# Kernel optimization log

Measured on AMD Instinct MI355X. Metric: run time of the kernel, lower is better.

Reference implementation:

```python
import jax, jax.numpy as jnp
import numpy as np

NUM_HEADS = 12
HEAD_CH = 64
WINDOW = 4


def _relative_to_absolute(x):
    # x: (B, H, L, 2L-1) -> (B, H, L, L) via skew trick
    B, H, L, _ = x.shape
    x = jnp.pad(x, ((0, 0), (0, 0), (0, 0), (0, 1)))        # (B,H,L,2L)
    x = x.reshape(B, H, L * 2 * L)
    x = jnp.pad(x, ((0, 0), (0, 0), (0, L - 1)))
    x = x.reshape(B, H, L + 1, 2 * L - 1)
    return x[:, :, :L, L - 1:]


def _get_relative_embeddings(emb, L):
    # emb: (H, 2W+1, D) -> (H, 2L-1, D)
    pad = max(0, L - WINDOW - 1)
    start = max(0, WINDOW - L + 1)
    e = jnp.pad(emb, ((0, 0), (pad, pad), (0, 0)))
    return e[:, start:start + 2 * L - 1, :]


def _forward(x, wq, bq, wk, bk, wv, bv, wo, bo, emb_rel_k, emb_rel_v):
    B, C, L = x.shape
    H, D = NUM_HEADS, HEAD_CH
    scale = 1.0 / np.sqrt(D).astype(np.float32)

    # 1x1 conv == channel matmul
    q = jnp.einsum('oc,bcl->bol', wq, x) + bq[None, :, None]
    k = jnp.einsum('oc,bcl->bol', wk, x) + bk[None, :, None]
    v = jnp.einsum('oc,bcl->bol', wv, x) + bv[None, :, None]

    # (B, C, L) -> (B, H, L, D)
    q = q.reshape(B, H, D, L).transpose(0, 1, 3, 2)
    k = k.reshape(B, H, D, L).transpose(0, 1, 3, 2)
    v = v.reshape(B, H, D, L).transpose(0, 1, 3, 2)

    score = jnp.einsum('bhld,bhmd->bhlm', q, k) * scale      # (B,H,L,L)

    rel_k = _get_relative_embeddings(emb_rel_k, L)           # (H, 2L-1, D)
    s_rel = jnp.einsum('bhld,hmd->bhlm', q, rel_k)           # (B,H,L,2L-1)
    score = score + _relative_to_absolute(s_rel) * scale

    attn = jax.nn.softmax(score, axis=-1)                    # dropout p=0 -> identity

    res = jnp.einsum('bhlm,bhmd->bhld', attn, v)             # (B,H,L,D)

    # absolute_to_relative skew
    a = jnp.pad(attn, ((0, 0), (0, 0), (0, 0), (0, L - 1)))
    a = a.reshape(B, H, L * (2 * L - 1))
    a = jnp.pad(a, ((0, 0), (0, 0), (L, 0)))
    rel_w = a.reshape(B, H, L, 2 * L)[:, :, :, 1:]           # (B,H,L,2L-1)

    rel_v = _get_relative_embeddings(emb_rel_v, L)           # (H, 2L-1, D)
    res = res + jnp.einsum('bhlm,hmd->bhld', rel_w, rel_v)

    res = res.transpose(0, 1, 3, 2).reshape(B, H * D, L)     # (B, C, L)
    out = jnp.einsum('oc,bcl->bol', wo, res) + bo[None, :, None]
    return out


def setup_inputs() -> dict:
    key = jax.random.key(0)
    ks = jax.random.split(key, 11)
    B, C, L = 4, 768, 1024
    rel_std = HEAD_CH ** (-0.5)
    xavier = np.sqrt(6.0 / (C + C)).astype(np.float32)
    return {
        'x': jax.random.normal(ks[0], (B, C, L), jnp.float32),
        'wq': jax.random.uniform(ks[1], (C, C), jnp.float32, -xavier, xavier),
        'bq': jnp.zeros((C,), jnp.float32),
        'wk': jax.random.uniform(ks[2], (C, C), jnp.float32, -xavier, xavier),
        'bk': jnp.zeros((C,), jnp.float32),
        'wv': jax.random.uniform(ks[3], (C, C), jnp.float32, -xavier, xavier),
        'bv': jnp.zeros((C,), jnp.float32),
        'wo': jax.random.normal(ks[4], (C, C), jnp.float32) * 0.02,
        'bo': jnp.zeros((C,), jnp.float32),
        'emb_rel_k': jax.random.normal(ks[5], (NUM_HEADS, 2 * WINDOW + 1, HEAD_CH), jnp.float32) * rel_std,
        'emb_rel_v': jax.random.normal(ks[6], (NUM_HEADS, 2 * WINDOW + 1, HEAD_CH), jnp.float32) * rel_std,
    }


def reference(x, wq, bq, wk, bk, wv, bv, wo, bo, emb_rel_k, emb_rel_v):
    return _forward(x, wq, bq, wk, bk, wv, bv, wo, bo, emb_rel_k, emb_rel_v)
```

## Files before the change

kernel.cpp:

```cpp
#include <hip/hip_runtime.h>

#define NB   4
#define NH   12
#define HD   64
#define CCH  768
#define LQ   1024
#define SCALE 0.125f
#define STAB  4.0f
#define WELE (CCH*CCH)

typedef unsigned short u16;
typedef __bf16 bf16x8 __attribute__((ext_vector_type(8)));
typedef unsigned short u16x8 __attribute__((ext_vector_type(8)));
typedef unsigned short u16x4 __attribute__((ext_vector_type(4)));
typedef float floatx4 __attribute__((ext_vector_type(4)));

__device__ __forceinline__ float bf2f(u16 u) {
    union { unsigned int i; float f; } x; x.i = ((unsigned int)u) << 16; return x.f;
}
__device__ __forceinline__ u16 f2bf_u(float f) {
    union { float f; unsigned int i; } x; x.f = f;
    unsigned int i = x.i;
    return (u16)((i + 0x7FFFu + ((i >> 16) & 1u)) >> 16);
}
__device__ __forceinline__ void glds16(const u16* g, u16* l) {
    __builtin_amdgcn_global_load_lds(
        (const __attribute__((address_space(1))) unsigned int*)g,
        (__attribute__((address_space(3))) unsigned int*)l, 16, 0, 0);
}

__global__ __launch_bounds__(256) void convert_w_kernel(
    const float* __restrict__ wq, const float* __restrict__ wk,
    const float* __restrict__ wv, const float* __restrict__ wo,
    u16* __restrict__ wb)
{
    const int p = blockIdx.y;
    const float* src = (p == 0) ? wq : (p == 1) ? wk : (p == 2) ? wv : wo;
    u16* dst = wb + (size_t)p * WELE;
    const int idx = (blockIdx.x * 256 + threadIdx.x) * 4;
    const float4 v = *reinterpret_cast<const float4*>(src + idx);
    u16x4 o;
    o[0] = f2bf_u(v.x); o[1] = f2bf_u(v.y); o[2] = f2bf_u(v.z); o[3] = f2bf_u(v.w);
    *reinterpret_cast<u16x4*>(dst + idx) = o;
}

__global__ __launch_bounds__(256) void transpose_x_kernel(
    const float* __restrict__ x, u16* __restrict__ xT)
{
    __shared__ u16 tile[64 * 68];
    const int l0 = blockIdx.x * 64, c0 = blockIdx.y * 64, b = blockIdx.z;
    const int t = threadIdx.x;
    const float* xb = x + (size_t)b * CCH * LQ;
    {
        const int l = t & 63, cg = t >> 6;
        for (int i = 0; i < 16; ++i) {
            const int c = cg * 16 + i;
            tile[c * 68 + l] = f2bf_u(xb[(size_t)(c0 + c) * LQ + l0 + l]);
        }
    }
    __syncthreads();
    {
        const int c = t & 63, lg = t >> 6;
        for (int i = 0; i < 16; ++i) {
            const int l = lg * 16 + i;
            xT[((size_t)b * LQ + l0 + l) * CCH + c0 + c] = tile[c * 68 + l];
        }
    }
}

#define GEMM_CORE(Ag, Bg)                                                     \
    __shared__ __align__(16) u16 a_tile[128 * 64];                            \
    __shared__ __align__(16) u16 b_tile[128 * 64];                            \
    const int t = threadIdx.x;                                                \
    const int wave = t >> 6, lane = t & 63;                                   \
    const int quad = lane >> 4, l16 = lane & 15;                              \
    const int wm = (wave >> 1) * 64, wn = (wave & 1) * 64;                    \
    floatx4 acc[4][4];                                                        \
    _Pragma("unroll") for (int mi = 0; mi < 4; ++mi)                          \
        _Pragma("unroll") for (int ni = 0; ni < 4; ++ni)                      \
            _Pragma("unroll") for (int r = 0; r < 4; ++r) acc[mi][ni][r] = 0.f;\
    for (int k0 = 0; k0 < CCH; k0 += 64) {                                    \
        __syncthreads();                                                      \
        _Pragma("unroll") for (int i = 0; i < 4; ++i) {                       \
            const int sbase = wave * 256 + i * 64;                            \
            const int s = sbase + lane;                                       \
            const int m = s >> 3, pos = s & 7;                                \
            const int gpos = pos ^ (m & 7);                                   \
            glds16(Ag + (size_t)(m0 + m) * CCH + k0 + gpos * 8,               \
                   &a_tile[sbase * 8]);                                       \
            glds16(Bg + (size_t)(n0 + m) * CCH + k0 + gpos * 8,               \
                   &b_tile[sbase * 8]);                                       \
        }                                                                     \
        __syncthreads();                                                      \
        bf16x8 af[2][4], bfr[2][4];                                           \
        _Pragma("unroll") for (int s = 0; s < 2; ++s)                         \
            _Pragma("unroll") for (int i = 0; i < 4; ++i) {                   \
                const int am = wm + i * 16 + l16;                             \
                const int bn = wn + i * 16 + l16;                             \
                const int c = s * 4 + quad;                                   \
                af[s][i]  = *reinterpret_cast<const bf16x8*>(                 \
                    &a_tile[(am * 8 + (c ^ (am & 7))) * 8]);                  \
                bfr[s][i] = *reinterpret_cast<const bf16x8*>(                 \
                    &b_tile[(bn * 8 + (c ^ (bn & 7))) * 8]);                  \
            }                                                                 \
        _Pragma("unroll") for (int s = 0; s < 2; ++s)                         \
            _Pragma("unroll") for (int mi = 0; mi < 4; ++mi)                  \
                _Pragma("unroll") for (int ni = 0; ni < 4; ++ni)              \
                    acc[mi][ni] = __builtin_amdgcn_mfma_f32_16x16x32_bf16(    \
                        af[s][mi], bfr[s][ni], acc[mi][ni], 0, 0, 0);         \
    }

__global__ __launch_bounds__(256) void proj_qkv_kernel(
    const u16* __restrict__ xT, const u16* __restrict__ wb,
    const float* __restrict__ bq, const float* __restrict__ bk,
    const float* __restrict__ bv,
    u16* __restrict__ Qw, u16* __restrict__ Kw, u16* __restrict__ Vw)
{
    const int z = blockIdx.z, b = z / 3, p = z % 3;
    const int n0 = blockIdx.x * 128, m0 = blockIdx.y * 128;
    const u16* Ag = wb + (size_t)p * WELE;
    const u16* Bg = xT + (size_t)b * LQ * CCH;
    const float* bias = (p == 0) ? bq : (p == 1) ? bk : bv;
    u16* Y = ((p == 0) ? Qw : (p == 1) ? Kw : Vw) + (size_t)b * CCH * LQ;

    GEMM_CORE(Ag, Bg)

#pragma unroll
    for (int mi = 0; mi < 4; ++mi) {
#pragma unroll
        for (int r = 0; r < 4; ++r) {
            const int o = m0 + wm + mi * 16 + quad * 4 + r;
            const float bb = bias[o];
#pragma unroll
            for (int ni = 0; ni < 4; ++ni) {
                const int l = n0 + wn + ni * 16 + l16;
                Y[(size_t)o * LQ + l] = f2bf_u(acc[mi][ni][r] + bb);
            }
        }
    }
}

__global__ __launch_bounds__(256) void proj_out_kernel(
    const u16* __restrict__ resb, const u16* __restrict__ wb,
    const float* __restrict__ bo, float* __restrict__ out)
{
    const int b = blockIdx.z;
    const int n0 = blockIdx.x * 128, m0 = blockIdx.y * 128;
    const u16* Ag = wb + (size_t)3 * WELE;
    const u16* Bg = resb + (size_t)b * LQ * CCH;
    float* Y = out + (size_t)b * CCH * LQ;

    GEMM_CORE(Ag, Bg)

#pragma unroll
    for (int mi = 0; mi < 4; ++mi) {
#pragma unroll
        for (int r = 0; r < 4; ++r) {
            const int o = m0 + wm + mi * 16 + quad * 4 + r;
            const float bb = bo[o];
#pragma unroll
            for (int ni = 0; ni < 4; ++ni) {
                const int l = n0 + wn + ni * 16 + l16;
                Y[(size_t)o * LQ + l] = acc[mi][ni][r] + bb;
            }
        }
    }
}

#define KSTRIDE 72

__global__ __launch_bounds__(256) void attn_kernel(
    const u16* __restrict__ Qw, const u16* __restrict__ Kw,
    const u16* __restrict__ Vw,
    const float* __restrict__ erk, const float* __restrict__ erv,
    u16* __restrict__ resb)
{
    __shared__ __align__(16) u16 kv_lds[2 * 64 * KSTRIDE];
    __shared__ __align__(16) u16 p_lds[4 * 16 * KSTRIDE];
    __shared__ float bias_lds[64 * 9];
    __shared__ float bandw_lds[64 * 9];
    __shared__ float erk_lds[9 * 64];
    __shared__ float erv_lds[9 * 64];

    u16* k16 = kv_lds;
    u16* v16 = kv_lds + 64 * KSTRIDE;
    u16* kdiag = kv_lds;

    const int t = threadIdx.x;
    const int wave = t >> 6, lane = t & 63;
    const int quad = lane >> 4, l16 = lane & 15;
    const int l0 = blockIdx.x * 64, h = blockIdx.y, b = blockIdx.z;
    const int rbase = wave * 16;
    const size_t base = ((size_t)b * CCH + (size_t)h * HD) * LQ;
    const u16* Qb = Qw + base;
    const u16* Kb = Kw + base;
    const u16* Vb = Vw + base;

    for (int i = t; i < 9 * 64; i += 256) {
        erk_lds[i] = erk[(size_t)h * 9 * 64 + i];
        erv_lds[i] = erv[(size_t)h * 9 * 64 + i];
    }

    bf16x8 qa0, qa1;
    {
        const int lg = l0 + rbase + l16;
        union { u16x8 u; bf16x8 v; } t0, t1;
#pragma unroll
        for (int jj = 0; jj < 8; ++jj) {
            t0.u[jj] = Qb[(size_t)(quad * 8 + jj) * LQ + lg];
            t1.u[jj] = Qb[(size_t)(32 + quad * 8 + jj) * LQ + lg];
        }
        qa0 = t0.v; qa1 = t1.v;
    }
    __syncthreads();

    {
        union { bf16x8 v; u16x8 u; } a0, a1; a0.v = qa0; a1.v = qa1;
        float qf[16];
#pragma unroll
        for (int jj = 0; jj < 8; ++jj) { qf[jj] = bf2f(a0.u[jj]); qf[8 + jj] = bf2f(a1.u[jj]); }
        for (int dl = 0; dl < 9; ++dl) {
            float s = 0.f;
#pragma unroll
            for (int jj = 0; jj < 8; ++jj) {
                s += qf[jj]     * erk_lds[dl * 64 + quad * 8 + jj];
                s += qf[8 + jj] * erk_lds[dl * 64 + 32 + quad * 8 + jj];
            }
            s += __shfl_xor(s, 16, 64);
            s += __shfl_xor(s, 32, 64);
            if (quad == 0) bias_lds[(rbase + l16) * 9 + dl] = s;
        }
    }

    floatx4 O[4];
    float l_acc = 0.f;
#pragma unroll
    for (int i = 0; i < 4; ++i)
#pragma unroll
        for (int r = 0; r < 4; ++r) O[i][r] = 0.f;

    u16* pw = p_lds + wave * 16 * KSTRIDE;
    const int qrow = rbase + l16;
    const int lgq = l0 + qrow;

    for (int kb = 0; kb < 16; ++kb) {
        const int j0 = kb * 64;
        __syncthreads();
        {
            u16 tmp[16];
#pragma unroll
            for (int dd = 0; dd < 16; ++dd)
                tmp[dd] = Kb[(size_t)(wave * 16 + dd) * LQ + j0 + lane];
            *reinterpret_cast<u16x8*>(&k16[lane * KSTRIDE + wave * 16])     = *reinterpret_cast<u16x8*>(tmp);
            *reinterpret_cast<u16x8*>(&k16[lane * KSTRIDE + wave * 16 + 8]) = *reinterpret_cast<u16x8*>(tmp + 8);
        }
        {
            const int d = t >> 2, seg = t & 3;
            const u16x8* src = reinterpret_cast<const u16x8*>(Vb + (size_t)d * LQ + j0 + seg * 16);
            *reinterpret_cast<u16x8*>(&v16[d * KSTRIDE + seg * 16])     = src[0];
            *reinterpret_cast<u16x8*>(&v16[d * KSTRIDE + seg * 16 + 8]) = src[1];
        }
        __syncthreads();

        floatx4 s4[4];
#pragma unroll
        for (int tt = 0; tt < 4; ++tt) {
            const bf16x8 ka0 = *reinterpret_cast<const bf16x8*>(&k16[(tt * 16 + l16) * KSTRIDE + quad * 8]);
            const bf16x8 ka1 = *reinterpret_cast<const bf16x8*>(&k16[(tt * 16 + l16) * KSTRIDE + 32 + quad * 8]);
            floatx4 c;
#pragma unroll
            for (int r = 0; r < 4; ++r) c[r] = 0.f;
            c = __builtin_amdgcn_mfma_f32_16x16x32_bf16(ka0, qa0, c, 0, 0, 0);
            c = __builtin_amdgcn_mfma_f32_16x16x32_bf16(ka1, qa1, c, 0, 0, 0);
            s4[tt] = c;
        }

        {
            const int lgmin = l0 + rbase, lgmax = lgmin + 15;
            if (j0 + 63 >= lgmin - 4 && j0 <= lgmax + 4) {
#pragma unroll
                for (int tt = 0; tt < 4; ++tt) {
#pragma unroll
                    for (int r = 0; r < 4; ++r) {
                        const int key = j0 + tt * 16 + quad * 4 + r;
                        const int delta = key - lgq + 4;
                        if (delta >= 0 && delta <= 8) s4[tt][r] += bias_lds[qrow * 9 + delta];
                    }
                }
            }
        }

#pragma unroll
        for (int tt = 0; tt < 4; ++tt) {
            u16x4 pk;
#pragma unroll
            for (int r = 0; r < 4; ++r) {
                const float p = __expf(fmaf(s4[tt][r], SCALE, -STAB));
                l_acc += p;
                pk[r] = f2bf_u(p);
            }
            *reinterpret_cast<u16x4*>(&pw[l16 * KSTRIDE + tt * 16 + quad * 4]) = pk;
        }

        const bf16x8 pa0 = *reinterpret_cast<const bf16x8*>(&pw[l16 * KSTRIDE + quad * 8]);
        const bf16x8 pa1 = *reinterpret_cast<const bf16x8*>(&pw[l16 * KSTRIDE + 32 + quad * 8]);
#pragma unroll
        for (int tt = 0; tt < 4; ++tt) {
            const bf16x8 vb0 = *reinterpret_cast<const bf16x8*>(&v16[(tt * 16 + l16) * KSTRIDE + quad * 8]);
            const bf16x8 vb1 = *reinterpret_cast<const bf16x8*>(&v16[(tt * 16 + l16) * KSTRIDE + 32 + quad * 8]);
            O[tt] = __builtin_amdgcn_mfma_f32_16x16x32_bf16(pa0, vb0, O[tt], 0, 0, 0);
            O[tt] = __builtin_amdgcn_mfma_f32_16x16x32_bf16(pa1, vb1, O[tt], 0, 0, 0);
        }
    }

    float l_tot = l_acc;
    l_tot += __shfl_xor(l_tot, 16, 64);
    l_tot += __shfl_xor(l_tot, 32, 64);

    __syncthreads();

    {
#pragma unroll
        for (int dd = 0; dd < 16; ++dd) {
            const int d = wave * 16 + dd;
            int j = l0 - 4 + lane;
            int jc = min(max(j, 0), LQ - 1);
            kdiag[lane * KSTRIDE + d] = Kb[(size_t)d * LQ + jc];
            if (lane < 8) {
                j = l0 + 60 + lane;
                jc = min(j, LQ - 1);
                kdiag[(64 + lane) * KSTRIDE + d] = Kb[(size_t)d * LQ + jc];
            }
        }
    }
    __syncthreads();

    {
        union { bf16x8 v; u16x8 u; } a0, a1; a0.v = qa0; a1.v = qa1;
        float qf[16];
#pragma unroll
        for (int jj = 0; jj < 8; ++jj) { qf[jj] = bf2f(a0.u[jj]); qf[8 + jj] = bf2f(a1.u[jj]); }
        for (int dl = 0; dl < 9; ++dl) {
            union { bf16x8 v; u16x8 u; } k0, k1;
            k0.v = *reinterpret_cast<const bf16x8*>(&kdiag[(qrow + dl) * KSTRIDE + quad * 8]);
            k1.v = *reinterpret_cast<const bf16x8*>(&kdiag[(qrow + dl) * KSTRIDE + 32 + quad * 8]);
            float s = 0.f;
#pragma unroll
            for (int jj = 0; jj < 8; ++jj) {
                s += qf[jj]     * bf2f(k0.u[jj]);
                s += qf[8 + jj] * bf2f(k1.u[jj]);
            }
            s += __shfl_xor(s, 16, 64);
            s += __shfl_xor(s, 32, 64);
            const int jgl = lgq + dl - 4;
            float pband = 0.f;
            if (jgl >= 0 && jgl < LQ)
                pband = __expf(fmaf(s + bias_lds[qrow * 9 + dl], SCALE, -STAB));
            if (quad == 0) bandw_lds[qrow * 9 + dl] = pband;
        }
    }

    float rinv[4];
#pragma unroll
    for (int r = 0; r < 4; ++r) {
        const int src = (lane & 48) | (quad * 4 + r);
        rinv[r] = 1.0f / __shfl(l_tot, src, 64);
    }

#pragma unroll
    for (int tt = 0; tt < 4; ++tt) {
#pragma unroll
        for (int r = 0; r < 4; ++r) {
            const int row = rbase + quad * 4 + r;
            const int d = tt * 16 + l16;
            float val = O[tt][r];
#pragma unroll
            for (int dl = 0; dl < 9; ++dl)
                val += bandw_lds[row * 9 + dl] * erv_lds[dl * 64 + d];
            val *= rinv[r];
            resb[((size_t)b * LQ + (l0 + row)) * CCH + h * HD + d] = f2bf_u(val);
        }
    }
}

extern "C" void kernel_launch(void* const* d_in, const int* in_sizes, int n_in,
                              void* d_out, int out_size, void* d_ws, size_t ws_size,
                              hipStream_t stream) {
    const float* x   = (const float*)d_in[0];
    const float* wq  = (const float*)d_in[1];
    const float* bq  = (const float*)d_in[2];
    const float* wk  = (const float*)d_in[3];
    const float* bk  = (const float*)d_in[4];
    const float* wv  = (const float*)d_in[5];
    const float* bv  = (const float*)d_in[6];
    const float* wo  = (const float*)d_in[7];
    const float* bo  = (const float*)d_in[8];
    const float* erk = (const float*)d_in[9];
    const float* erv = (const float*)d_in[10];
    float* out = (float*)d_out;

    const size_t NEL = (size_t)NB * CCH * LQ;
    u16* xT   = (u16*)d_ws;
    u16* wb   = xT + NEL;
    u16* Qw   = wb + (size_t)4 * WELE;
    u16* Kw   = Qw + NEL;
    u16* Vw   = Kw + NEL;
    u16* resb = Vw + NEL;

    convert_w_kernel<<<dim3(WELE / 1024, 4), 256, 0, stream>>>(wq, wk, wv, wo, wb);
    transpose_x_kernel<<<dim3(16, 12, 4), 256, 0, stream>>>(x, xT);
    proj_qkv_kernel<<<dim3(8, 6, 12), 256, 0, stream>>>(
        xT, wb, bq, bk, bv, Qw, Kw, Vw);
    attn_kernel<<<dim3(LQ / 64, NH, NB), 256, 0, stream>>>(
        Qw, Kw, Vw, erk, erv, resb);
    proj_out_kernel<<<dim3(8, 6, 4), 256, 0, stream>>>(resb, wb, bo, out);
}
```

Measured before the change: 194.0 us.

## Store K token-major and load MFMA fragments directly from global memory

The QKV projection now writes K transposed (L x C) by swapping GEMM operands for the K slice. The attention kernel can then read K fragments straight from global memory into registers, with no LDS staging and no per-element gather. V tiles are register-prefetched one block ahead, the diagonal K band is read directly from global, and expf is replaced by exp2 with pre-scaled constants. This drops the LDS transpose work and one barrier pair. In exchange it adds more global loads per wave and changes the store pattern of the K projection epilogue, which becomes a strided per-element write.

```diff
diff --git a/kernel.cpp b/kernel.cpp
--- a/kernel.cpp
+++ b/kernel.cpp
@@ -7,6 +7,8 @@
 #define LQ   1024
 #define SCALE 0.125f
 #define STAB  4.0f
+#define SC2  0.18033688f
+#define ST2  5.7707802f
 #define WELE (CCH*CCH)
 
 typedef unsigned short u16;
@@ -117,24 +119,50 @@
     u16* __restrict__ Qw, u16* __restrict__ Kw, u16* __restrict__ Vw)
 {
     const int z = blockIdx.z, b = z / 3, p = z % 3;
-    const int n0 = blockIdx.x * 128, m0 = blockIdx.y * 128;
-    const u16* Ag = wb + (size_t)p * WELE;
-    const u16* Bg = xT + (size_t)b * LQ * CCH;
-    const float* bias = (p == 0) ? bq : (p == 1) ? bk : bv;
-    u16* Y = ((p == 0) ? Qw : (p == 1) ? Kw : Vw) + (size_t)b * CCH * LQ;
+    int m0, n0;
+    const u16 *Ag, *Bg;
+    if (p == 1) {
+        m0 = blockIdx.x * 128;
+        n0 = blockIdx.y * 128;
+        Ag = xT + (size_t)b * LQ * CCH;
+        Bg = wb + (size_t)WELE;
+    } else {
+        n0 = blockIdx.x * 128;
+        m0 = blockIdx.y * 128;
+        Ag = wb + (size_t)p * WELE;
+        Bg = xT + (size_t)b * LQ * CCH;
+    }
 
     GEMM_CORE(Ag, Bg)
 
-#pragma unroll
-    for (int mi = 0; mi < 4; ++mi) {
-#pragma unroll
-        for (int r = 0; r < 4; ++r) {
-            const int o = m0 + wm + mi * 16 + quad * 4 + r;
-            const float bb = bias[o];
-#pragma unroll
-            for (int ni = 0; ni < 4; ++ni) {
-                const int l = n0 + wn + ni * 16 + l16;
-                Y[(size_t)o * LQ + l] = f2bf_u(acc[mi][ni][r] + bb);
+    if (p == 1) {
+        u16* Y = Kw + (size_t)b * LQ * CCH;
+#pragma unroll
+        for (int mi = 0; mi < 4; ++mi) {
+#pragma unroll
+            for (int r = 0; r < 4; ++r) {
+                const int l = m0 + wm + mi * 16 + quad * 4 + r;
+#pragma unroll
+                for (int ni = 0; ni < 4; ++ni) {
+                    const int o = n0 + wn + ni * 16 + l16;
+                    Y[(size_t)l * CCH + o] = f2bf_u(acc[mi][ni][r] + bk[o]);
+                }
+            }
+        }
+    } else {
+        const float* bias = (p == 0) ? bq : bv;
+        u16* Y = ((p == 0) ? Qw : Vw) + (size_t)b * CCH * LQ;
+#pragma unroll
+        for (int mi = 0; mi < 4; ++mi) {
+#pragma unroll
+            for (int r = 0; r < 4; ++r) {
+                const int o = m0 + wm + mi * 16 + quad * 4 + r;
+                const float bb = bias[o];
+#pragma unroll
+                for (int ni = 0; ni < 4; ++ni) {
+                    const int l = n0 + wn + ni * 16 + l16;
+                    Y[(size_t)o * LQ + l] = f2bf_u(acc[mi][ni][r] + bb);
+                }
             }
         }
     }
@@ -170,21 +198,17 @@
 #define KSTRIDE 72
 
 __global__ __launch_bounds__(256) void attn_kernel(
-    const u16* __restrict__ Qw, const u16* __restrict__ Kw,
+    const u16* __restrict__ Qw, const u16* __restrict__ Kt,
     const u16* __restrict__ Vw,
     const float* __restrict__ erk, const float* __restrict__ erv,
     u16* __restrict__ resb)
 {
-    __shared__ __align__(16) u16 kv_lds[2 * 64 * KSTRIDE];
+    __shared__ __align__(16) u16 v16[64 * KSTRIDE];
     __shared__ __align__(16) u16 p_lds[4 * 16 * KSTRIDE];
     __shared__ float bias_lds[64 * 9];
     __shared__ float bandw_lds[64 * 9];
     __shared__ float erk_lds[9 * 64];
     __shared__ float erv_lds[9 * 64];
-
-    u16* k16 = kv_lds;
-    u16* v16 = kv_lds + 64 * KSTRIDE;
-    u16* kdiag = kv_lds;
 
     const int t = threadIdx.x;
     const int wave = t >> 6, lane = t & 63;
@@ -193,8 +217,8 @@
     const int rbase = wave * 16;
     const size_t base = ((size_t)b * CCH + (size_t)h * HD) * LQ;
     const u16* Qb = Qw + base;
-    const u16* Kb = Kw + base;
     const u16* Vb = Vw + base;
+    const u16* Kb = Kt + (size_t)b * LQ * CCH + (size_t)h * HD;
 
     for (int i = t; i < 9 * 64; i += 256) {
         erk_lds[i] = erk[(size_t)h * 9 * 64 + i];
@@ -232,6 +256,13 @@
         }
     }
 
+    const int vd = t >> 2, vseg = t & 3;
+    u16x8 vp0, vp1;
+    {
+        const u16x8* src = reinterpret_cast<const u16x8*>(Vb + (size_t)vd * LQ + vseg * 16);
+        vp0 = src[0]; vp1 = src[1];
+    }
+
     floatx4 O[4];
     float l_acc = 0.f;
 #pragma unroll
@@ -245,33 +276,34 @@
 
     for (int kb = 0; kb < 16; ++kb) {
         const int j0 = kb * 64;
+
+        bf16x8 ka[4][2];
+#pragma unroll
+        for (int tt = 0; tt < 4; ++tt) {
+            const u16* kr = Kb + (size_t)(j0 + tt * 16 + l16) * CCH;
+            ka[tt][0] = *reinterpret_cast<const bf16x8*>(kr + quad * 8);
+            ka[tt][1] = *reinterpret_cast<const bf16x8*>(kr + 32 + quad * 8);
+        }
+
         __syncthreads();
+        *reinterpret_cast<u16x8*>(&v16[vd * KSTRIDE + vseg * 16])     = vp0;
+        *reinterpret_cast<u16x8*>(&v16[vd * KSTRIDE + vseg * 16 + 8]) = vp1;
+        __syncthreads();
+
         {
-            u16 tmp[16];
-#pragma unroll
-            for (int dd = 0; dd < 16; ++dd)
-                tmp[dd] = Kb[(size_t)(wave * 16 + dd) * LQ + j0 + lane];
-            *reinterpret_cast<u16x8*>(&k16[lane * KSTRIDE + wave * 16])     = *reinterpret_cast<u16x8*>(tmp);
-            *reinterpret_cast<u16x8*>(&k16[lane * KSTRIDE + wave * 16 + 8]) = *reinterpret_cast<u16x8*>(tmp + 8);
-        }
-        {
-            const int d = t >> 2, seg = t & 3;
-            const u16x8* src = reinterpret_cast<const u16x8*>(Vb + (size_t)d * LQ + j0 + seg * 16);
-            *reinterpret_cast<u16x8*>(&v16[d * KSTRIDE + seg * 16])     = src[0];
-            *reinterpret_cast<u16x8*>(&v16[d * KSTRIDE + seg * 16 + 8]) = src[1];
-        }
-        __syncthreads();
+            const int nj0 = (kb < 15) ? j0 + 64 : j0;
+            const u16x8* src = reinterpret_cast<const u16x8*>(Vb + (size_t)vd * LQ + nj0 + vseg * 16);
+            vp0 = src[0]; vp1 = src[1];
+        }
 
         floatx4 s4[4];
 #pragma unroll
         for (int tt = 0; tt < 4; ++tt) {
-            const bf16x8 ka0 = *reinterpret_cast<const bf16x8*>(&k16[(tt * 16 + l16) * KSTRIDE + quad * 8]);
-            const bf16x8 ka1 = *reinterpret_cast<const bf16x8*>(&k16[(tt * 16 + l16) * KSTRIDE + 32 + quad * 8]);
             floatx4 c;
 #pragma unroll
             for (int r = 0; r < 4; ++r) c[r] = 0.f;
-            c = __builtin_amdgcn_mfma_f32_16x16x32_bf16(ka0, qa0, c, 0, 0, 0);
-            c = __builtin_amdgcn_mfma_f32_16x16x32_bf16(ka1, qa1, c, 0, 0, 0);
+            c = __builtin_amdgcn_mfma_f32_16x16x32_bf16(ka[tt][0], qa0, c, 0, 0, 0);
+            c = __builtin_amdgcn_mfma_f32_16x16x32_bf16(ka[tt][1], qa1, c, 0, 0, 0);
             s4[tt] = c;
         }
 
@@ -295,7 +327,7 @@
             u16x4 pk;
 #pragma unroll
             for (int r = 0; r < 4; ++r) {
-                const float p = __expf(fmaf(s4[tt][r], SCALE, -STAB));
+                const float p = __builtin_amdgcn_exp2f(fmaf(s4[tt][r], SC2, -ST2));
                 l_acc += p;
                 pk[r] = f2bf_u(p);
             }
@@ -317,33 +349,18 @@
     l_tot += __shfl_xor(l_tot, 16, 64);
     l_tot += __shfl_xor(l_tot, 32, 64);
 
-    __syncthreads();
-
-    {
-#pragma unroll
-        for (int dd = 0; dd < 16; ++dd) {
-            const int d = wave * 16 + dd;
-            int j = l0 - 4 + lane;
-            int jc = min(max(j, 0), LQ - 1);
-            kdiag[lane * KSTRIDE + d] = Kb[(size_t)d * LQ + jc];
-            if (lane < 8) {
-                j = l0 + 60 + lane;
-                jc = min(j, LQ - 1);
-                kdiag[(64 + lane) * KSTRIDE + d] = Kb[(size_t)d * LQ + jc];
-            }
-        }
-    }
-    __syncthreads();
-
     {
         union { bf16x8 v; u16x8 u; } a0, a1; a0.v = qa0; a1.v = qa1;
         float qf[16];
 #pragma unroll
         for (int jj = 0; jj < 8; ++jj) { qf[jj] = bf2f(a0.u[jj]); qf[8 + jj] = bf2f(a1.u[jj]); }
         for (int dl = 0; dl < 9; ++dl) {
+            const int jgl = lgq + dl - 4;
+            const int jc = min(max(jgl, 0), LQ - 1);
+            const u16* kr = Kb + (size_t)jc * CCH;
             union { bf16x8 v; u16x8 u; } k0, k1;
-            k0.v = *reinterpret_cast<const bf16x8*>(&kdiag[(qrow + dl) * KSTRIDE + quad * 8]);
-            k1.v = *reinterpret_cast<const bf16x8*>(&kdiag[(qrow + dl) * KSTRIDE + 32 + quad * 8]);
+            k0.v = *reinterpret_cast<const bf16x8*>(kr + quad * 8);
+            k1.v = *reinterpret_cast<const bf16x8*>(kr + 32 + quad * 8);
             float s = 0.f;
 #pragma unroll
             for (int jj = 0; jj < 8; ++jj) {
@@ -352,10 +369,9 @@
             }
             s += __shfl_xor(s, 16, 64);
             s += __shfl_xor(s, 32, 64);
-            const int jgl = lgq + dl - 4;
             float pband = 0.f;
             if (jgl >= 0 && jgl < LQ)
-                pband = __expf(fmaf(s + bias_lds[qrow * 9 + dl], SCALE, -STAB));
+                pband = __builtin_amdgcn_exp2f(fmaf(s + bias_lds[qrow * 9 + dl], SC2, -ST2));
             if (quad == 0) bandw_lds[qrow * 9 + dl] = pband;
         }
     }
```

After: 216.2 us. +11.4%, slower.
